# Kernel tuning notes

Measured on AMD Instinct MI355X. Metric: run time of the kernel, lower is better.

## Reference

```python
import jax, jax.numpy as jnp
import numpy as np

IMPOSSIBLE = -10000000.0
NUM_LABELS = 10
NUM_TAGS = 1 + 4 * NUM_LABELS  # 41
B, T = 4096, 256


def _bioul_constraints(num_labels):
    O, I, Bt, L, U = 0, 1, 2, 3, 4
    n = 1 + 4 * num_labels
    ft = np.ones((n, n), dtype=bool)
    ft[O, O] = False
    for i in range(num_labels):
        S = 4 * i
        for j in range(num_labels):
            SJ = 4 * j
            ft[L + S, Bt + SJ] = False
            ft[L + S, U + SJ] = False
            ft[U + S, Bt + SJ] = False
            ft[U + S, U + SJ] = False
        ft[O, Bt + S] = False
        ft[Bt + S, I + S] = False
        ft[I + S, I + S] = False
        ft[I + S, L + S] = False
        ft[Bt + S, L + S] = False
        ft[L + S, O] = False
        ft[O, U + S] = False
        ft[U + S, O] = False
    sft = np.zeros(n, dtype=bool)
    eft = np.zeros(n, dtype=bool)
    for i in range(num_labels):
        S = 4 * i
        sft[I + S] = True   # cannot start inside an entity
        sft[L + S] = True
        eft[I + S] = True   # cannot end inside an entity
        eft[Bt + S] = True
    return jnp.asarray(ft), jnp.asarray(sft), jnp.asarray(eft)


def setup_inputs() -> dict:
    key = jax.random.key(0)
    k1, k2, k3, k4, k5 = jax.random.split(key, 5)
    emissions = jax.random.normal(k1, (B, T, NUM_TAGS), dtype=jnp.float32)
    # left-aligned valid prefixes, as required by masked_flip semantics
    lengths = jax.random.randint(k2, (B,), T // 2, T + 1)
    mask = jnp.arange(T)[None, :] < lengths[:, None]
    # gold path: everything tagged O (tag 0) -- a valid BIOUL sequence
    target = jnp.zeros((B, T, NUM_TAGS), dtype=bool).at[:, :, 0].set(True)
    transitions = jax.random.normal(k3, (NUM_TAGS, NUM_TAGS), dtype=jnp.float32) * 0.1
    start_transitions = jax.random.normal(k4, (NUM_TAGS,), dtype=jnp.float32) * 0.1
    end_transitions = jax.random.normal(k5, (NUM_TAGS,), dtype=jnp.float32) * 0.1
    ft, sft, eft = _bioul_constraints(NUM_LABELS)
    return {
        "emissions": emissions,
        "mask": mask,
        "target": target,
        "transitions": transitions,
        "start_transitions": start_transitions,
        "end_transitions": end_transitions,
        "forbidden_transitions": ft,
        "start_forbidden_transitions": sft,
        "end_forbidden_transitions": eft,
    }


def _crf_loss(emissions, mask, target, transitions, start_transitions,
              end_transitions, ft, sft, eft):
    trans = jnp.where(ft, IMPOSSIBLE, transitions)           # [n, n]
    start = jnp.where(sft, IMPOSSIBLE, start_transitions)    # [n]
    end = jnp.where(eft, IMPOSSIBLE, end_transitions)        # [n]
    # supervised (target-restricted) and unsupervised emission scores
    sup = jnp.where(target, emissions, IMPOSSIBLE)           # [B, T, n]
    bi = jnp.stack([sup, emissions], axis=1)                 # [B, 2, T, n]
    bi = jnp.swapaxes(bi, 0, 2)                              # [T, 2, B, n]
    init = bi[0] + start                                     # [2, B, n]

    def step(prev, e_k):
        # logsumexp_reduce: alpha'[j] = logsumexp_i(alpha[i] + trans[i, j]) + e_k[j]
        nxt = jax.nn.logsumexp(prev[..., :, None] + trans, axis=-2) + e_k
        return nxt, nxt

    _, outs = jax.lax.scan(step, init, bi[1:])
    out = jnp.concatenate([init[None], outs], axis=0)        # [T, 2, B, n]
    out = jnp.swapaxes(out, 0, 2)                            # [B, 2, T, n]
    # masked_flip(...)[:, :, 0] == alpha at the last valid token
    lengths = mask.sum(-1)                                   # [B]
    idx = (lengths - 1)[:, None, None, None]
    z = jnp.take_along_axis(out, idx, axis=2)[:, :, 0] + end # [B, 2, n]
    supervised_z = jax.nn.logsumexp(z[:, 0], axis=-1)
    unsupervised_z = jax.nn.logsumexp(z[:, 1], axis=-1)
    return -(supervised_z - unsupervised_z)                  # [B]


def reference(emissions, mask, target, transitions, start_transitions,
              end_transitions, forbidden_transitions,
              start_forbidden_transitions, end_forbidden_transitions):
    return _crf_loss(emissions, mask, target, transitions, start_transitions,
                     end_transitions, forbidden_transitions,
                     start_forbidden_transitions, end_forbidden_transitions)
```

## Files before the change

### kernel.cpp

```cpp
#include <hip/hip_runtime.h>
#include <stdint.h>

#define NT 41
#define TT 256

typedef __attribute__((ext_vector_type(8))) short short8;
typedef __attribute__((ext_vector_type(16))) float f32x16;
typedef __attribute__((ext_vector_type(2))) int int2v;

union FragU { short8 s; uint32_t u[4]; };

static __device__ __forceinline__ uint32_t pk_bf16(float lo, float hi) {
    uint32_t d;
    asm("v_cvt_pk_bf16_f32 %0, %1, %2" : "=v"(d) : "v"(lo), "v"(hi));
    return d;
}
static __device__ __forceinline__ float asf(int x){ return __builtin_bit_cast(float, x); }
static __device__ __forceinline__ int   asi(float x){ return __builtin_bit_cast(int, x); }

static __device__ __forceinline__ float hsum(float x) {
    int2v r = __builtin_amdgcn_permlane32_swap(asi(x), asi(x), false, false);
    return asf(r[0]) + asf(r[1]);
}
static __device__ __forceinline__ uint32_t dpp_pairswap(uint32_t v) {
    return (uint32_t)__builtin_amdgcn_update_dpp(0, (int)v, 0xB1, 0xF, 0xF, true);
}
static __device__ __forceinline__ uint32_t u4c(uint4 v, int q) {
    return q==0 ? v.x : q==1 ? v.y : q==2 ? v.z : v.w;
}
static __device__ __forceinline__ short8 packB(const float* g) {
    FragU u;
    u.u[0] = pk_bf16(g[0], g[1]); u.u[1] = pk_bf16(g[2], g[3]);
    u.u[2] = pk_bf16(g[4], g[5]); u.u[3] = pk_bf16(g[6], g[7]);
    return u.s;
}

template<bool BYTE>
static __device__ __forceinline__ uint32_t bAt(const void* p, size_t idx) {
    if (BYTE) return (uint32_t)((const uint8_t*)p)[idx];
    return (((const uint32_t*)p)[idx] != 0u) ? 1u : 0u;
}

static __device__ __forceinline__ int rowOf(int rr, int h) {
    return (rr < 16) ? ((rr & 3) + 8 * (rr >> 2) + 4 * h)
                     : (32 + ((rr - 16) & 3) + 8 * ((rr - 16) >> 2) + 4 * h);
}

template<bool BYTE>
static __device__ void run_all(const float* __restrict__ em, const void* __restrict__ maskp,
    const void* __restrict__ tgtp, const float* __restrict__ trans,
    const float* __restrict__ st, const float* __restrict__ en,
    const void* __restrict__ ftp, const void* __restrict__ sftp,
    const void* __restrict__ eftp, float* __restrict__ out)
{
    __shared__ float sB[21][64];
    __shared__ float sLb[64];

    const int tid  = threadIdx.x;
    const int wid  = tid >> 6;
    const int lane = tid & 63;
    const int c = lane & 31;
    const int h = lane >> 5;
    const int bbase = blockIdx.x * 16;
    const int b = bbase + (c >> 1);
    const bool sup = ((c & 1) == 0);
    const size_t eb0 = (size_t)b * TT * NT;

    int len = 0;
    if (BYTE) {
        const uint8_t* mr = (const uint8_t*)maskp + (size_t)b * TT;
        #pragma unroll
        for (int k = 0; k < 16; ++k) {
            uint4 v; __builtin_memcpy(&v, mr + k*16, 16);
            len += __popc(v.x)+__popc(v.y)+__popc(v.z)+__popc(v.w);
        }
    } else {
        const uint32_t* mr = (const uint32_t*)maskp + (size_t)b * TT;
        for (int k = 0; k < TT; k += 4) {
            uint4 v; __builtin_memcpy(&v, mr + k, 16);
            len += (v.x!=0)+(v.y!=0)+(v.z!=0)+(v.w!=0);
        }
    }
    int tm = len;
    #pragma unroll
    for (int o = 1; o < 64; o <<= 1) { int t2 = __shfl_xor(tm, o); tm = t2 > tm ? t2 : tm; }

    float w[3][21];
    uint4 S[3][5]; uint32_t S40[3];
    const char* myrow = sup ? (const char*)(em + eb0)
                            : (const char*)tgtp + eb0 * 4;

    auto issueSlot = [&](int sl, int t) {
        const char* rp = myrow + (size_t)t * (NT * 4);
        #pragma unroll
        for (int m = 0; m < 5; ++m) {
            const int off = 4 * ((m < 4) ? (8*m + 4*h) : (32 + 4*h));
            uint4 tmp; __builtin_memcpy(&tmp, rp + off, 16);
            S[sl][m] = tmp;
        }
        uint32_t t40; __builtin_memcpy(&t40, rp + 160, 4);
        S40[sl] = t40;
    };
    auto convSlot = [&](int sl) {
        #pragma unroll
        for (int rr = 0; rr < 21; ++rr) {
            uint32_t mine = (rr < 20) ? u4c(S[sl][rr>>2], rr & 3) : S40[sl];
            uint32_t oth  = dpp_pairswap(mine);
            uint32_t embits = sup ? mine : oth;
            uint32_t tgbits = sup ? oth  : mine;
            float e = __expf(__builtin_bit_cast(float, embits));
            w[sl][rr] = ((!sup) || (tgbits != 0u)) ? e : 0.0f;
        }
    };
    auto loadStageB = [&](int s, int t) {
        const float* base = em + eb0 + (size_t)t * NT;
        float ev[21];
        #pragma unroll
        for (int m = 0; m < 5; ++m) {
            const int off = (m < 4) ? (8*m + 4*h) : (32 + 4*h);
            float4 tmp; __builtin_memcpy(&tmp, base + off, 16);
            ev[4*m+0]=tmp.x; ev[4*m+1]=tmp.y; ev[4*m+2]=tmp.z; ev[4*m+3]=tmp.w;
        }
        ev[20] = base[40];
        const uint32_t om = sup ? 0u : 0x01010101u;
        uint32_t tw[5]; uint32_t t40;
        const uint8_t* tb = (const uint8_t*)tgtp + eb0 + (size_t)t * NT;
        #pragma unroll
        for (int m = 0; m < 5; ++m) {
            const int off = (m < 4) ? (8*m + 4*h) : (32 + 4*h);
            uint32_t w_; __builtin_memcpy(&w_, tb + off, 4);
            tw[m] = w_ | om;
        }
        t40 = (((uint32_t)tb[40]) | om) & 0xffu;
        #pragma unroll
        for (int rr = 0; rr < 20; ++rr)
            w[s][rr] = __expf(ev[rr]) * (float)((tw[rr>>2] >> (8*(rr&3))) & 0xffu);
        w[s][20] = __expf(ev[20]) * (float)t40;
    };

    float aD[21];
    float logSf = 0.0f;
    const f32x16 z16 = (f32x16)0.0f;

    if (wid == 0) {
        short8 A0[3], A1[3];
        #pragma unroll
        for (int mb = 0; mb < 2; ++mb)
        #pragma unroll
        for (int ch = 0; ch < 3; ++ch) {
            float v[8];
            #pragma unroll
            for (int e = 0; e < 8; ++e) {
                const int src = (e&3) + 8*(e>>2) + 4*h + 16*ch;
                const int j = mb*32 + c;
                float val = 0.0f;
                if (src < NT && j < NT && bAt<BYTE>(ftp, src*NT + j) == 0u)
                    val = __expf(trans[src*NT + j]);
                v[e] = val;
            }
            FragU u; u.u[0]=pk_bf16(v[0],v[1]); u.u[1]=pk_bf16(v[2],v[3]);
            u.u[2]=pk_bf16(v[4],v[5]); u.u[3]=pk_bf16(v[6],v[7]);
            if (mb==0) A0[ch]=u.s; else A1[ch]=u.s;
        }

        #pragma unroll
        for (int rr = 0; rr < 21; ++rr) {
            const int row = rowOf(rr, h);
            float val = 0.0f;
            if (row < NT) {
                float wv = __expf(em[eb0 + row]);
                if (sup) wv *= (bAt<BYTE>(tgtp, eb0 + row) ? 1.0f : 0.0f);
                const float se = (bAt<BYTE>(sftp, row) == 0u) ? __expf(st[row]) : 0.0f;
                val = wv * se;
            }
            aD[rr] = val;
        }
        short8 B0 = packB(aD+0), B1 = packB(aD+8);
        short8 B2;
        { float tl[8] = {aD[16],aD[17],aD[18],aD[19],aD[20],0,0,0}; B2 = packB(tl); }

        if (BYTE) { loadStageB(0,1); loadStageB(1,2); loadStageB(2,3); }
        else      { issueSlot(0,1); issueSlot(1,2); issueSlot(2,3); convSlot(0); }

        for (int tb = 1; tb <= 127; tb += 3) {
            #pragma unroll
            for (int s = 0; s < 3; ++s) {
                const int t = tb + s;
                if (t <= 127) {
                    if (!BYTE) issueSlot(s, t + 3);
                    f32x16 d0 = __builtin_amdgcn_mfma_f32_32x32x16_bf16(A0[0], B0, z16, 0,0,0);
                    d0 = __builtin_amdgcn_mfma_f32_32x32x16_bf16(A0[1], B1, d0, 0,0,0);
                    d0 = __builtin_amdgcn_mfma_f32_32x32x16_bf16(A0[2], B2, d0, 0,0,0);
                    f32x16 d1 = __builtin_amdgcn_mfma_f32_32x32x16_bf16(A1[0], B0, z16, 0,0,0);
                    d1 = __builtin_amdgcn_mfma_f32_32x32x16_bf16(A1[1], B1, d1, 0,0,0);
                    d1 = __builtin_amdgcn_mfma_f32_32x32x16_bf16(A1[2], B2, d1, 0,0,0);
                    #pragma unroll
                    for (int rr = 0; rr < 16; ++rr) aD[rr] = d0[rr] * w[s][rr];
                    #pragma unroll
                    for (int rr = 0; rr < 4; ++rr) aD[16+rr] = d1[rr] * w[s][16+rr];
                    aD[20] = d1[4] * w[s][20];
                    if ((t & 7) == 0) {
                        float cs = 0.0f;
                        #pragma unroll
                        for (int rr = 0; rr < 21; ++rr) cs += aD[rr];
                        cs = hsum(cs); cs = fmaxf(cs, 1e-30f);
                        const float rinv = 1.0f / cs;
                        logSf += __logf(cs);
                        #pragma unroll
                        for (int rr = 0; rr < 21; ++rr) aD[rr] *= rinv;
                    }
                    B0 = packB(aD+0); B1 = packB(aD+8);
                    float tl[8] = {aD[16],aD[17],aD[18],aD[19],aD[20],0,0,0};
                    B2 = packB(tl);
                    if (BYTE) loadStageB(s, t + 3);
                    else      convSlot((s + 1) % 3);
                }
            }
        }
    } else {
        short8 A0[3], A1[3];
        #pragma unroll
        for (int mb = 0; mb < 2; ++mb)
        #pragma unroll
        for (int ch = 0; ch < 3; ++ch) {
            float v[8];
            #pragma unroll
            for (int e = 0; e < 8; ++e) {
                const int src = (e&3) + 8*(e>>2) + 4*h + 16*ch;
                const int i = mb*32 + c;
                float val = 0.0f;
                if (src < NT && i < NT && bAt<BYTE>(ftp, i*NT + src) == 0u)
                    val = __expf(trans[i*NT + src]);
                v[e] = val;
            }
            FragU u; u.u[0]=pk_bf16(v[0],v[1]); u.u[1]=pk_bf16(v[2],v[3]);
            u.u[2]=pk_bf16(v[4],v[5]); u.u[3]=pk_bf16(v[6],v[7]);
            if (mb==0) A0[ch]=u.s; else A1[ch]=u.s;
        }

        float endD[21];
        #pragma unroll
        for (int rr = 0; rr < 21; ++rr) {
            const int row = rowOf(rr, h);
            endD[rr] = (row < NT && bAt<BYTE>(eftp, row) == 0u) ? __expf(en[row]) : 0.0f;
        }

        short8 G0 = {0,0,0,0,0,0,0,0}, G1 = {0,0,0,0,0,0,0,0}, G2 = {0,0,0,0,0,0,0,0};
        float logSb = 0.0f;

        if (BYTE) { loadStageB(0, tm-1); loadStageB(1, tm-2); loadStageB(2, tm-3); }
        else      { issueSlot(0, tm-1); issueSlot(1, tm-2); issueSlot(2, tm-3); convSlot(0); }

        for (int tb = tm - 1; tb >= 128; tb -= 3) {
            #pragma unroll
            for (int s = 0; s < 3; ++s) {
                const int t = tb - s;
                if (t >= 128) {
                    if (!BYTE) issueSlot(s, t - 3);
                    f32x16 d0 = __builtin_amdgcn_mfma_f32_32x32x16_bf16(A0[0], G0, z16, 0,0,0);
                    d0 = __builtin_amdgcn_mfma_f32_32x32x16_bf16(A0[1], G1, d0, 0,0,0);
                    d0 = __builtin_amdgcn_mfma_f32_32x32x16_bf16(A0[2], G2, d0, 0,0,0);
                    f32x16 d1 = __builtin_amdgcn_mfma_f32_32x32x16_bf16(A1[0], G0, z16, 0,0,0);
                    d1 = __builtin_amdgcn_mfma_f32_32x32x16_bf16(A1[1], G1, d1, 0,0,0);
                    d1 = __builtin_amdgcn_mfma_f32_32x32x16_bf16(A1[2], G2, d1, 0,0,0);
                    const bool sel = (len - 1 == t);
                    float gD[21];
                    #pragma unroll
                    for (int rr = 0; rr < 16; ++rr) gD[rr] = (sel ? endD[rr] : d0[rr]) * w[s][rr];
                    #pragma unroll
                    for (int rr = 0; rr < 4; ++rr) gD[16+rr] = (sel ? endD[16+rr] : d1[rr]) * w[s][16+rr];
                    gD[20] = (sel ? endD[20] : d1[4]) * w[s][20];
                    if ((t & 7) == 0) {
                        float cs = 0.0f;
                        #pragma unroll
                        for (int rr = 0; rr < 21; ++rr) cs += gD[rr];
                        cs = hsum(cs);
                        const bool started = (len - 1 >= t);
                        const float csc = fmaxf(cs, 1e-30f);
                        const float rinv = started ? (1.0f / csc) : 1.0f;
                        logSb += started ? __logf(csc) : 0.0f;
                        #pragma unroll
                        for (int rr = 0; rr < 21; ++rr) gD[rr] *= rinv;
                    }
                    G0 = packB(gD+0); G1 = packB(gD+8);
                    float tl[8] = {gD[16],gD[17],gD[18],gD[19],gD[20],0,0,0};
                    G2 = packB(tl);
                    if (BYTE) loadStageB(s, t - 3);
                    else      convSlot((s + 1) % 3);
                }
            }
        }

        f32x16 d0 = __builtin_amdgcn_mfma_f32_32x32x16_bf16(A0[0], G0, z16, 0,0,0);
        d0 = __builtin_amdgcn_mfma_f32_32x32x16_bf16(A0[1], G1, d0, 0,0,0);
        d0 = __builtin_amdgcn_mfma_f32_32x32x16_bf16(A0[2], G2, d0, 0,0,0);
        f32x16 d1 = __builtin_amdgcn_mfma_f32_32x32x16_bf16(A1[0], G0, z16, 0,0,0);
        d1 = __builtin_amdgcn_mfma_f32_32x32x16_bf16(A1[1], G1, d1, 0,0,0);
        d1 = __builtin_amdgcn_mfma_f32_32x32x16_bf16(A1[2], G2, d1, 0,0,0);
        const bool sel = (len - 1 == 127);
        #pragma unroll
        for (int rr = 0; rr < 16; ++rr) sB[rr][lane] = sel ? endD[rr] : d0[rr];
        #pragma unroll
        for (int rr = 0; rr < 4; ++rr) sB[16+rr][lane] = sel ? endD[16+rr] : d1[rr];
        sB[20][lane] = sel ? endD[20] : d1[4];
        sLb[lane] = logSb;
    }

    __syncthreads();

    if (wid == 0) {
        float es = 0.0f;
        #pragma unroll
        for (int rr = 0; rr < 21; ++rr) es = fmaf(aD[rr], sB[rr][lane], es);
        es = hsum(es);
        const float zc = __logf(fmaxf(es, 1e-37f)) + logSf + sLb[lane];
        const float zo = __shfl_xor(zc, 1);
        if ((lane & 1) == 0 && lane < 32)
            out[bbase + (lane >> 1)] = zo - zc;
    }
}

__global__ __launch_bounds__(128, 1) void crf_fb(
    const float* __restrict__ em, const void* __restrict__ maskp,
    const void* __restrict__ tgtp, const float* __restrict__ trans,
    const float* __restrict__ st, const float* __restrict__ en,
    const void* __restrict__ ftp, const void* __restrict__ sftp,
    const void* __restrict__ eftp, float* __restrict__ out)
{
    const bool byteMode = (*(const uint32_t*)maskp == 0x01010101u);
    if (byteMode) run_all<true >(em, maskp, tgtp, trans, st, en, ftp, sftp, eftp, out);
    else          run_all<false>(em, maskp, tgtp, trans, st, en, ftp, sftp, eftp, out);
}

extern "C" void kernel_launch(void* const* d_in, const int* in_sizes, int n_in,
                              void* d_out, int out_size, void* d_ws, size_t ws_size,
                              hipStream_t stream) {
    const float* em    = (const float*)d_in[0];
    const void*  maskp = d_in[1];
    const void*  tgtp  = d_in[2];
    const float* trans = (const float*)d_in[3];
    const float* st    = (const float*)d_in[4];
    const float* en    = (const float*)d_in[5];
    const void*  ftp   = d_in[6];
    const void*  sftp  = d_in[7];
    const void*  eftp  = d_in[8];
    float* out = (float*)d_out;

    crf_fb<<<4096 / 16, 128, 0, stream>>>(em, maskp, tgtp, trans, st, en,
                                          ftp, sftp, eftp, out);
}
```

Before: 128.0 us.

## Stage emission/target prefetch through LDS via global_load_lds instead of registers

Replaces the register-held three-slot prefetch of emission and target rows with direct global-to-LDS loads into a four-slot shared-memory ring per wave, tracked with explicit vmcnt waits. Each step reads its slot from LDS and computes the exp weights just before the MFMA chain rather than after it. This is meant to cut VGPR pressure from the in-flight prefetch buffers and the per-slot weight arrays. In exchange it adds LDS traffic and depends on a hand-counted vmcnt threshold, and the byte path now loads synchronously inside the step instead of being prefetched three steps ahead.

```diff
diff --git a/kernel.cpp b/kernel.cpp
--- a/kernel.cpp
+++ b/kernel.cpp
@@ -3,6 +3,7 @@
 
 #define NT 41
 #define TT 256
+#define SLOT_U4 336
 
 typedef __attribute__((ext_vector_type(8))) short short8;
 typedef __attribute__((ext_vector_type(16))) float f32x16;
@@ -24,9 +25,6 @@
 }
 static __device__ __forceinline__ uint32_t dpp_pairswap(uint32_t v) {
     return (uint32_t)__builtin_amdgcn_update_dpp(0, (int)v, 0xB1, 0xF, 0xF, true);
-}
-static __device__ __forceinline__ uint32_t u4c(uint4 v, int q) {
-    return q==0 ? v.x : q==1 ? v.y : q==2 ? v.z : v.w;
 }
 static __device__ __forceinline__ short8 packB(const float* g) {
     FragU u;
@@ -53,6 +51,7 @@
     const void* __restrict__ ftp, const void* __restrict__ sftp,
     const void* __restrict__ eftp, float* __restrict__ out)
 {
+    __shared__ uint4 stage[2][4][SLOT_U4];
     __shared__ float sB[21][64];
     __shared__ float sLb[64];
 
@@ -85,34 +84,51 @@
     #pragma unroll
     for (int o = 1; o < 64; o <<= 1) { int t2 = __shfl_xor(tm, o); tm = t2 > tm ? t2 : tm; }
 
-    float w[3][21];
-    uint4 S[3][5]; uint32_t S40[3];
     const char* myrow = sup ? (const char*)(em + eb0)
                             : (const char*)tgtp + eb0 * 4;
+    uint4* mystage = &stage[wid][0][0];
 
     auto issueSlot = [&](int sl, int t) {
         const char* rp = myrow + (size_t)t * (NT * 4);
+        uint4* slotb = mystage + sl * SLOT_U4;
         #pragma unroll
         for (int m = 0; m < 5; ++m) {
             const int off = 4 * ((m < 4) ? (8*m + 4*h) : (32 + 4*h));
-            uint4 tmp; __builtin_memcpy(&tmp, rp + off, 16);
-            S[sl][m] = tmp;
-        }
-        uint32_t t40; __builtin_memcpy(&t40, rp + 160, 4);
-        S40[sl] = t40;
+            __builtin_amdgcn_global_load_lds(
+                (const __attribute__((address_space(1))) uint32_t*)(rp + off),
+                (__attribute__((address_space(3))) uint32_t*)(slotb + m * 64),
+                16, 0, 0);
+        }
+        __builtin_amdgcn_global_load_lds(
+            (const __attribute__((address_space(1))) uint32_t*)(rp + 160),
+            (__attribute__((address_space(3))) uint32_t*)((uint32_t*)slotb + 1280),
+            4, 0, 0);
     };
-    auto convSlot = [&](int sl) {
+
+    uint32_t mine[21];
+    auto ldSlot = [&](int sl) {
+        asm volatile("s_waitcnt vmcnt(12)" ::: "memory");
+        __builtin_amdgcn_sched_barrier(0);
+        const uint4* slotb = mystage + sl * SLOT_U4;
+        #pragma unroll
+        for (int m = 0; m < 5; ++m) {
+            uint4 v = slotb[m * 64 + lane];
+            mine[4*m+0]=v.x; mine[4*m+1]=v.y; mine[4*m+2]=v.z; mine[4*m+3]=v.w;
+        }
+        mine[20] = ((const uint32_t*)slotb)[1280 + lane];
+    };
+    float w[21];
+    auto mkW = [&]() {
         #pragma unroll
         for (int rr = 0; rr < 21; ++rr) {
-            uint32_t mine = (rr < 20) ? u4c(S[sl][rr>>2], rr & 3) : S40[sl];
-            uint32_t oth  = dpp_pairswap(mine);
-            uint32_t embits = sup ? mine : oth;
-            uint32_t tgbits = sup ? oth  : mine;
+            uint32_t oth = dpp_pairswap(mine[rr]);
+            uint32_t embits = sup ? mine[rr] : oth;
+            uint32_t tgbits = sup ? oth : mine[rr];
             float e = __expf(__builtin_bit_cast(float, embits));
-            w[sl][rr] = ((!sup) || (tgbits != 0u)) ? e : 0.0f;
+            w[rr] = ((!sup) || (tgbits != 0u)) ? e : 0.0f;
         }
     };
-    auto loadStageB = [&](int s, int t) {
+    auto loadStageB = [&](int t) {
         const float* base = em + eb0 + (size_t)t * NT;
         float ev[21];
         #pragma unroll
@@ -134,8 +150,8 @@
         t40 = (((uint32_t)tb[40]) | om) & 0xffu;
         #pragma unroll
         for (int rr = 0; rr < 20; ++rr)
-            w[s][rr] = __expf(ev[rr]) * (float)((tw[rr>>2] >> (8*(rr&3))) & 0xffu);
-        w[s][20] = __expf(ev[20]) * (float)t40;
+            w[rr] = __expf(ev[rr]) * (float)((tw[rr>>2] >> (8*(rr&3))) & 0xffu);
+        w[20] = __expf(ev[20]) * (float)t40;
     };
 
     float aD[21];
@@ -163,6 +179,8 @@
             if (mb==0) A0[ch]=u.s; else A1[ch]=u.s;
         }
 
+        if (!BYTE) { issueSlot(1 & 3, 1); issueSlot(2 & 3, 2); issueSlot(3 & 3, 3); }
+
         #pragma unroll
         for (int rr = 0; rr < 21; ++rr) {
             const int row = rowOf(rr, h);
@@ -179,15 +197,18 @@
         short8 B2;
         { float tl[8] = {aD[16],aD[17],aD[18],aD[19],aD[20],0,0,0}; B2 = packB(tl); }
 
-        if (BYTE) { loadStageB(0,1); loadStageB(1,2); loadStageB(2,3); }
-        else      { issueSlot(0,1); issueSlot(1,2); issueSlot(2,3); convSlot(0); }
-
         for (int tb = 1; tb <= 127; tb += 3) {
             #pragma unroll
             for (int s = 0; s < 3; ++s) {
                 const int t = tb + s;
                 if (t <= 127) {
-                    if (!BYTE) issueSlot(s, t + 3);
+                    if (!BYTE) {
+                        ldSlot(t & 3);
+                        issueSlot((t + 3) & 3, t + 3);
+                        mkW();
+                    } else {
+                        loadStageB(t);
+                    }
                     f32x16 d0 = __builtin_amdgcn_mfma_f32_32x32x16_bf16(A0[0], B0, z16, 0,0,0);
                     d0 = __builtin_amdgcn_mfma_f32_32x32x16_bf16(A0[1], B1, d0, 0,0,0);
                     d0 = __builtin_amdgcn_mfma_f32_32x32x16_bf16(A0[2], B2, d0, 0,0,0);
@@ -195,10 +216,10 @@
                     d1 = __builtin_amdgcn_mfma_f32_32x32x16_bf16(A1[1], B1, d1, 0,0,0);
                     d1 = __builtin_amdgcn_mfma_f32_32x32x16_bf16(A1[2], B2, d1, 0,0,0);
                     #pragma unroll
-                    for (int rr = 0; rr < 16; ++rr) aD[rr] = d0[rr] * w[s][rr];
+                    for (int rr = 0; rr < 16; ++rr) aD[rr] = d0[rr] * w[rr];
                     #pragma unroll
-                    for (int rr = 0; rr < 4; ++rr) aD[16+rr] = d1[rr] * w[s][16+rr];
-                    aD[20] = d1[4] * w[s][20];
+                    for (int rr = 0; rr < 4; ++rr) aD[16+rr] = d1[rr] * w[16+rr];
+                    aD[20] = d1[4] * w[20];
                     if ((t & 7) == 0) {
                         float cs = 0.0f;
                         #pragma unroll
@@ -212,8 +233,6 @@
                     B0 = packB(aD+0); B1 = packB(aD+8);
                     float tl[8] = {aD[16],aD[17],aD[18],aD[19],aD[20],0,0,0};
                     B2 = packB(tl);
-                    if (BYTE) loadStageB(s, t + 3);
-                    else      convSlot((s + 1) % 3);
                 }
             }
         }
@@ -248,15 +267,20 @@
         short8 G0 = {0,0,0,0,0,0,0,0}, G1 = {0,0,0,0,0,0,0,0}, G2 = {0,0,0,0,0,0,0,0};
         float logSb = 0.0f;
 
-        if (BYTE) { loadStageB(0, tm-1); loadStageB(1, tm-2); loadStageB(2, tm-3); }
-        else      { issueSlot(0, tm-1); issueSlot(1, tm-2); issueSlot(2, tm-3); convSlot(0); }
+        if (!BYTE) { issueSlot((tm-1) & 3, tm-1); issueSlot((tm-2) & 3, tm-2); issueSlot((tm-3) & 3, tm-3); }
 
         for (int tb = tm - 1; tb >= 128; tb -= 3) {
             #pragma unroll
             for (int s = 0; s < 3; ++s) {
                 const int t = tb - s;
                 if (t >= 128) {
-                    if (!BYTE) issueSlot(s, t - 3);
+                    if (!BYTE) {
+                        ldSlot(t & 3);
+                        issueSlot((t - 3) & 3, t - 3);
+                        mkW();
+                    } else {
+                        loadStageB(t);
+                    }
                     f32x16 d0 = __builtin_amdgcn_mfma_f32_32x32x16_bf16(A0[0], G0, z16, 0,0,0);
                     d0 = __builtin_amdgcn_mfma_f32_32x32x16_bf16(A0[1], G1, d0, 0,0,0);
                     d0 = __builtin_amdgcn_mfma_f32_32x32x16_bf16(A0[2], G2, d0, 0,0,0);
@@ -266,10 +290,10 @@
                     const bool sel = (len - 1 == t);
                     float gD[21];
                     #pragma unroll
-                    for (int rr = 0; rr < 16; ++rr) gD[rr] = (sel ? endD[rr] : d0[rr]) * w[s][rr];
+                    for (int rr = 0; rr < 16; ++rr) gD[rr] = (sel ? endD[rr] : d0[rr]) * w[rr];
                     #pragma unroll
-                    for (int rr = 0; rr < 4; ++rr) gD[16+rr] = (sel ? endD[16+rr] : d1[rr]) * w[s][16+rr];
-                    gD[20] = (sel ? endD[20] : d1[4]) * w[s][20];
+                    for (int rr = 0; rr < 4; ++rr) gD[16+rr] = (sel ? endD[16+rr] : d1[rr]) * w[16+rr];
+                    gD[20] = (sel ? endD[20] : d1[4]) * w[20];
                     if ((t & 7) == 0) {
                         float cs = 0.0f;
                         #pragma unroll
@@ -285,8 +309,6 @@
                     G0 = packB(gD+0); G1 = packB(gD+8);
                     float tl[8] = {gD[16],gD[17],gD[18],gD[19],gD[20],0,0,0};
                     G2 = packB(tl);
-                    if (BYTE) loadStageB(s, t - 3);
-                    else      convSlot((s + 1) % 3);
                 }
             }
         }
```

Result: slower. 137.3 us (+7.3%).

## Split CRF recurrence into six parallel time segments combined by matrix products

Applied to the files above, without the earlier changes.

Replaces the two-wave forward/backward split of the 256-step recurrence with six waves, each running a 64-step segment. Some waves propagate state vectors and others propagate ones-vectors through transfer products. A final combine step stitches the segment results together using dot products and one extra MFMA, with a branch per length bucket. The goal is to shorten the serial dependency chain per batch group from about 128 steps to about 64. The cost is more total work, more waves per block, extra register pressure and a more complex combine with different bf16 rounding behavior.

```diff
diff --git a/kernel.cpp b/kernel.cpp
--- a/kernel.cpp
+++ b/kernel.cpp
@@ -17,7 +17,6 @@
 }
 static __device__ __forceinline__ float asf(int x){ return __builtin_bit_cast(float, x); }
 static __device__ __forceinline__ int   asi(float x){ return __builtin_bit_cast(int, x); }
-
 static __device__ __forceinline__ float hsum(float x) {
     int2v r = __builtin_amdgcn_permlane32_swap(asi(x), asi(x), false, false);
     return asf(r[0]) + asf(r[1]);
@@ -28,22 +27,175 @@
 static __device__ __forceinline__ uint32_t u4c(uint4 v, int q) {
     return q==0 ? v.x : q==1 ? v.y : q==2 ? v.z : v.w;
 }
-static __device__ __forceinline__ short8 packB(const float* g) {
+static __device__ __forceinline__ short8 packB8(const float* g) {
     FragU u;
     u.u[0] = pk_bf16(g[0], g[1]); u.u[1] = pk_bf16(g[2], g[3]);
     u.u[2] = pk_bf16(g[4], g[5]); u.u[3] = pk_bf16(g[6], g[7]);
     return u.s;
 }
-
+static __device__ __forceinline__ short8 packTail(const float* g) {
+    float tl[8] = {g[0], g[1], g[2], g[3], g[4], 0.f, 0.f, 0.f};
+    return packB8(tl);
+}
 template<bool BYTE>
 static __device__ __forceinline__ uint32_t bAt(const void* p, size_t idx) {
     if (BYTE) return (uint32_t)((const uint8_t*)p)[idx];
     return (((const uint32_t*)p)[idx] != 0u) ? 1u : 0u;
 }
-
 static __device__ __forceinline__ int rowOf(int rr, int h) {
     return (rr < 16) ? ((rr & 3) + 8 * (rr >> 2) + 4 * h)
                      : (32 + ((rr - 16) & 3) + 8 * ((rr - 16) >> 2) + 4 * h);
+}
+static __device__ __forceinline__ void mfma6(const short8* A, short8 B0, short8 B1, short8 B2,
+                                             float* d ) {
+    const f32x16 z16 = (f32x16)0.0f;
+    f32x16 d0 = __builtin_amdgcn_mfma_f32_32x32x16_bf16(A[0], B0, z16, 0,0,0);
+    d0 = __builtin_amdgcn_mfma_f32_32x32x16_bf16(A[1], B1, d0, 0,0,0);
+    d0 = __builtin_amdgcn_mfma_f32_32x32x16_bf16(A[2], B2, d0, 0,0,0);
+    f32x16 d1 = __builtin_amdgcn_mfma_f32_32x32x16_bf16(A[3], B0, z16, 0,0,0);
+    d1 = __builtin_amdgcn_mfma_f32_32x32x16_bf16(A[4], B1, d1, 0,0,0);
+    d1 = __builtin_amdgcn_mfma_f32_32x32x16_bf16(A[5], B2, d1, 0,0,0);
+    #pragma unroll
+    for (int rr = 0; rr < 16; ++rr) d[rr] = d0[rr];
+    #pragma unroll
+    for (int rr = 0; rr < 5; ++rr) d[16+rr] = d1[rr];
+}
+
+template<bool BYTE>
+static __device__ void buildA(bool fwd, int c, int h, const float* trans,
+                              const void* ftp, short8* A) {
+    #pragma unroll
+    for (int mb = 0; mb < 2; ++mb)
+    #pragma unroll
+    for (int ch = 0; ch < 3; ++ch) {
+        float v[8];
+        #pragma unroll
+        for (int e = 0; e < 8; ++e) {
+            const int src = (e&3) + 8*(e>>2) + 4*h + 16*ch;
+            const int o = mb*32 + c;
+            const int i_ = fwd ? src : o;
+            const int j_ = fwd ? o : src;
+            float val = 0.0f;
+            if (src < NT && o < NT && bAt<BYTE>(ftp, i_*NT + j_) == 0u)
+                val = __expf(trans[i_*NT + j_]);
+            v[e] = val;
+        }
+        FragU u; u.u[0]=pk_bf16(v[0],v[1]); u.u[1]=pk_bf16(v[2],v[3]);
+        u.u[2]=pk_bf16(v[4],v[5]); u.u[3]=pk_bf16(v[6],v[7]);
+        A[mb*3 + ch] = u.s;
+    }
+}
+
+template<bool BYTE, int N, bool ASC, bool PRE, bool REINIT>
+static __device__ float run_pass(int t0, int len, bool sup, int h,
+    const char* myrow, const float* emb, const uint8_t* tgb8,
+    const short8* A, const float* endD, float aD[21])
+{
+    float w[3][21];
+    uint4 S[3][5]; uint32_t S40[3];
+
+    auto tAt = [&](int i){ return ASC ? (t0 + i) : (t0 - i); };
+    auto issueSlot = [&](int sl, int t) {
+        const char* rp = myrow + (size_t)t * (NT * 4);
+        #pragma unroll
+        for (int m = 0; m < 5; ++m) {
+            const int off = 4 * ((m < 4) ? (8*m + 4*h) : (32 + 4*h));
+            uint4 tmp; __builtin_memcpy(&tmp, rp + off, 16);
+            S[sl][m] = tmp;
+        }
+        uint32_t t40; __builtin_memcpy(&t40, rp + 160, 4);
+        S40[sl] = t40;
+    };
+    auto convSlot = [&](int sl) {
+        #pragma unroll
+        for (int rr = 0; rr < 21; ++rr) {
+            uint32_t mine = (rr < 20) ? u4c(S[sl][rr>>2], rr & 3) : S40[sl];
+            uint32_t oth = dpp_pairswap(mine);
+            uint32_t embits = sup ? mine : oth;
+            uint32_t tgbits = sup ? oth : mine;
+            float e = __expf(__builtin_bit_cast(float, embits));
+            w[sl][rr] = ((!sup) || (tgbits != 0u)) ? e : 0.0f;
+        }
+    };
+    auto loadB = [&](int sl, int t) {
+        const float* base = emb + (size_t)t * NT;
+        const uint8_t* tb = tgb8 + (size_t)t * NT;
+        const uint32_t om = sup ? 0u : 0x01010101u;
+        float ev[21]; uint32_t tw[5]; uint32_t t40;
+        #pragma unroll
+        for (int m = 0; m < 5; ++m) {
+            const int off = (m < 4) ? (8*m + 4*h) : (32 + 4*h);
+            float4 tmp; __builtin_memcpy(&tmp, base + off, 16);
+            ev[4*m+0]=tmp.x; ev[4*m+1]=tmp.y; ev[4*m+2]=tmp.z; ev[4*m+3]=tmp.w;
+            uint32_t w_; __builtin_memcpy(&w_, tb + off, 4);
+            tw[m] = w_ | om;
+        }
+        ev[20] = base[40];
+        t40 = (((uint32_t)tb[40]) | om) & 0xffu;
+        #pragma unroll
+        for (int rr = 0; rr < 20; ++rr)
+            w[sl][rr] = __expf(ev[rr]) * (float)((tw[rr>>2] >> (8*(rr&3))) & 0xffu);
+        w[sl][20] = __expf(ev[20]) * (float)t40;
+    };
+
+    if (!BYTE) {
+        issueSlot(0, tAt(0)); issueSlot(1, tAt(1)); issueSlot(2, tAt(2));
+        convSlot(0);
+    } else {
+        loadB(0, tAt(0));
+    }
+
+    float logS = 0.0f;
+    constexpr int NB3 = (N + 2) / 3;
+    for (int bb = 0; bb < NB3; ++bb) {
+        #pragma unroll
+        for (int s = 0; s < 3; ++s) {
+            const int i = bb * 3 + s;
+            if (i < N) {
+                if (!BYTE) { if (i + 3 < N) issueSlot(s, tAt(i + 3)); }
+                const int t = tAt(i);
+                short8 B0, B1, B2;
+                if (PRE) {
+                    float tmp[21];
+                    #pragma unroll
+                    for (int rr = 0; rr < 21; ++rr) tmp[rr] = aD[rr] * w[s][rr];
+                    B0 = packB8(tmp); B1 = packB8(tmp+8); B2 = packTail(tmp+16);
+                } else {
+                    B0 = packB8(aD); B1 = packB8(aD+8); B2 = packTail(aD+16);
+                }
+                float d[21]; mfma6(A, B0, B1, B2, d);
+                if (PRE) {
+                    #pragma unroll
+                    for (int rr = 0; rr < 21; ++rr) aD[rr] = d[rr];
+                } else if (REINIT) {
+                    const bool sel = (len - 1 == t);
+                    #pragma unroll
+                    for (int rr = 0; rr < 21; ++rr)
+                        aD[rr] = (sel ? endD[rr] : d[rr]) * w[s][rr];
+                } else {
+                    #pragma unroll
+                    for (int rr = 0; rr < 21; ++rr) aD[rr] = d[rr] * w[s][rr];
+                }
+                if ((t & 7) == 0) {
+                    const bool started = (!REINIT) || (len - 1 >= t);
+                    float cs = 0.0f;
+                    #pragma unroll
+                    for (int rr = 0; rr < 21; ++rr) cs += aD[rr];
+                    cs = hsum(cs);
+                    const float csc = fmaxf(cs, 1e-30f);
+                    const float rinv = started ? (1.0f / csc) : 1.0f;
+                    logS += started ? __logf(csc) : 0.0f;
+                    #pragma unroll
+                    for (int rr = 0; rr < 21; ++rr) aD[rr] *= rinv;
+                }
+                if (i + 1 < N) {
+                    if (BYTE) loadB((s + 1) % 3, tAt(i + 1));
+                    else      convSlot((s + 1) % 3);
+                }
+            }
+        }
+    }
+    return logS;
 }
 
 template<bool BYTE>
@@ -53,8 +205,8 @@
     const void* __restrict__ ftp, const void* __restrict__ sftp,
     const void* __restrict__ eftp, float* __restrict__ out)
 {
-    __shared__ float sB[21][64];
-    __shared__ float sLb[64];
+    __shared__ float sb[6][21][64];
+    __shared__ float ssig[6][64];
 
     const int tid  = threadIdx.x;
     const int wid  = tid >> 6;
@@ -81,88 +233,29 @@
             len += (v.x!=0)+(v.y!=0)+(v.z!=0)+(v.w!=0);
         }
     }
-    int tm = len;
-    #pragma unroll
-    for (int o = 1; o < 64; o <<= 1) { int t2 = __shfl_xor(tm, o); tm = t2 > tm ? t2 : tm; }
-
-    float w[3][21];
-    uint4 S[3][5]; uint32_t S40[3];
+
     const char* myrow = sup ? (const char*)(em + eb0)
                             : (const char*)tgtp + eb0 * 4;
-
-    auto issueSlot = [&](int sl, int t) {
-        const char* rp = myrow + (size_t)t * (NT * 4);
-        #pragma unroll
-        for (int m = 0; m < 5; ++m) {
-            const int off = 4 * ((m < 4) ? (8*m + 4*h) : (32 + 4*h));
-            uint4 tmp; __builtin_memcpy(&tmp, rp + off, 16);
-            S[sl][m] = tmp;
-        }
-        uint32_t t40; __builtin_memcpy(&t40, rp + 160, 4);
-        S40[sl] = t40;
-    };
-    auto convSlot = [&](int sl) {
-        #pragma unroll
-        for (int rr = 0; rr < 21; ++rr) {
-            uint32_t mine = (rr < 20) ? u4c(S[sl][rr>>2], rr & 3) : S40[sl];
-            uint32_t oth  = dpp_pairswap(mine);
-            uint32_t embits = sup ? mine : oth;
-            uint32_t tgbits = sup ? oth  : mine;
-            float e = __expf(__builtin_bit_cast(float, embits));
-            w[sl][rr] = ((!sup) || (tgbits != 0u)) ? e : 0.0f;
-        }
-    };
-    auto loadStageB = [&](int s, int t) {
-        const float* base = em + eb0 + (size_t)t * NT;
-        float ev[21];
-        #pragma unroll
-        for (int m = 0; m < 5; ++m) {
-            const int off = (m < 4) ? (8*m + 4*h) : (32 + 4*h);
-            float4 tmp; __builtin_memcpy(&tmp, base + off, 16);
-            ev[4*m+0]=tmp.x; ev[4*m+1]=tmp.y; ev[4*m+2]=tmp.z; ev[4*m+3]=tmp.w;
-        }
-        ev[20] = base[40];
-        const uint32_t om = sup ? 0u : 0x01010101u;
-        uint32_t tw[5]; uint32_t t40;
-        const uint8_t* tb = (const uint8_t*)tgtp + eb0 + (size_t)t * NT;
-        #pragma unroll
-        for (int m = 0; m < 5; ++m) {
-            const int off = (m < 4) ? (8*m + 4*h) : (32 + 4*h);
-            uint32_t w_; __builtin_memcpy(&w_, tb + off, 4);
-            tw[m] = w_ | om;
-        }
-        t40 = (((uint32_t)tb[40]) | om) & 0xffu;
-        #pragma unroll
-        for (int rr = 0; rr < 20; ++rr)
-            w[s][rr] = __expf(ev[rr]) * (float)((tw[rr>>2] >> (8*(rr&3))) & 0xffu);
-        w[s][20] = __expf(ev[20]) * (float)t40;
-    };
+    const float*  emb  = em + eb0;
+    const uint8_t* tgb8 = (const uint8_t*)tgtp + eb0;
+
+    const bool isFwdA = (wid == 0 || wid == 1 || wid == 5);
+    short8 A[6];
+    buildA<BYTE>(isFwdA, c, h, trans, ftp, A);
+
+    float endD[21];
+    if (wid == 3 || wid == 4) {
+        #pragma unroll
+        for (int rr = 0; rr < 21; ++rr) {
+            const int row = rowOf(rr, h);
+            endD[rr] = (row < NT && bAt<BYTE>(eftp, row) == 0u) ? __expf(en[row]) : 0.0f;
+        }
+    }
 
     float aD[21];
-    float logSf = 0.0f;
-    const f32x16 z16 = (f32x16)0.0f;
+    float sig = 0.0f;
 
     if (wid == 0) {
-        short8 A0[3], A1[3];
-        #pragma unroll
-        for (int mb = 0; mb < 2; ++mb)
-        #pragma unroll
-        for (int ch = 0; ch < 3; ++ch) {
-            float v[8];
-            #pragma unroll
-            for (int e = 0; e < 8; ++e) {
-                const int src = (e&3) + 8*(e>>2) + 4*h + 16*ch;
-                const int j = mb*32 + c;
-                float val = 0.0f;
-                if (src < NT && j < NT && bAt<BYTE>(ftp, src*NT + j) == 0u)
-                    val = __expf(trans[src*NT + j]);
-                v[e] = val;
-            }
-            FragU u; u.u[0]=pk_bf16(v[0],v[1]); u.u[1]=pk_bf16(v[2],v[3]);
-            u.u[2]=pk_bf16(v[4],v[5]); u.u[3]=pk_bf16(v[6],v[7]);
-            if (mb==0) A0[ch]=u.s; else A1[ch]=u.s;
-        }
-
         #pragma unroll
         for (int rr = 0; rr < 21; ++rr) {
             const int row = rowOf(rr, h);
@@ -175,152 +268,82 @@
             }
             aD[rr] = val;
         }
-        short8 B0 = packB(aD+0), B1 = packB(aD+8);
-        short8 B2;
-        { float tl[8] = {aD[16],aD[17],aD[18],aD[19],aD[20],0,0,0}; B2 = packB(tl); }
-
-        if (BYTE) { loadStageB(0,1); loadStageB(1,2); loadStageB(2,3); }
-        else      { issueSlot(0,1); issueSlot(1,2); issueSlot(2,3); convSlot(0); }
-
-        for (int tb = 1; tb <= 127; tb += 3) {
-            #pragma unroll
-            for (int s = 0; s < 3; ++s) {
-                const int t = tb + s;
-                if (t <= 127) {
-                    if (!BYTE) issueSlot(s, t + 3);
-                    f32x16 d0 = __builtin_amdgcn_mfma_f32_32x32x16_bf16(A0[0], B0, z16, 0,0,0);
-                    d0 = __builtin_amdgcn_mfma_f32_32x32x16_bf16(A0[1], B1, d0, 0,0,0);
-                    d0 = __builtin_amdgcn_mfma_f32_32x32x16_bf16(A0[2], B2, d0, 0,0,0);
-                    f32x16 d1 = __builtin_amdgcn_mfma_f32_32x32x16_bf16(A1[0], B0, z16, 0,0,0);
-                    d1 = __builtin_amdgcn_mfma_f32_32x32x16_bf16(A1[1], B1, d1, 0,0,0);
-                    d1 = __builtin_amdgcn_mfma_f32_32x32x16_bf16(A1[2], B2, d1, 0,0,0);
-                    #pragma unroll
-                    for (int rr = 0; rr < 16; ++rr) aD[rr] = d0[rr] * w[s][rr];
-                    #pragma unroll
-                    for (int rr = 0; rr < 4; ++rr) aD[16+rr] = d1[rr] * w[s][16+rr];
-                    aD[20] = d1[4] * w[s][20];
-                    if ((t & 7) == 0) {
-                        float cs = 0.0f;
-                        #pragma unroll
-                        for (int rr = 0; rr < 21; ++rr) cs += aD[rr];
-                        cs = hsum(cs); cs = fmaxf(cs, 1e-30f);
-                        const float rinv = 1.0f / cs;
-                        logSf += __logf(cs);
-                        #pragma unroll
-                        for (int rr = 0; rr < 21; ++rr) aD[rr] *= rinv;
-                    }
-                    B0 = packB(aD+0); B1 = packB(aD+8);
-                    float tl[8] = {aD[16],aD[17],aD[18],aD[19],aD[20],0,0,0};
-                    B2 = packB(tl);
-                    if (BYTE) loadStageB(s, t + 3);
-                    else      convSlot((s + 1) % 3);
-                }
-            }
-        }
+        sig = run_pass<BYTE,63,true,false,false>(1, len, sup, h, myrow, emb, tgb8, A, endD, aD);
+    } else if (wid == 1) {
+        #pragma unroll
+        for (int rr = 0; rr < 21; ++rr) aD[rr] = (rowOf(rr,h) < NT) ? 1.0f : 0.0f;
+        sig = run_pass<BYTE,64,true,false,false>(64, len, sup, h, myrow, emb, tgb8, A, endD, aD);
+    } else if (wid == 2) {
+        #pragma unroll
+        for (int rr = 0; rr < 21; ++rr) aD[rr] = (rowOf(rr,h) < NT) ? 1.0f : 0.0f;
+        sig = run_pass<BYTE,64,false,true,false>(127, len, sup, h, myrow, emb, tgb8, A, endD, aD);
+    } else if (wid == 3) {
+        #pragma unroll
+        for (int rr = 0; rr < 21; ++rr) aD[rr] = 0.0f;
+        sig = run_pass<BYTE,64,false,false,true>(255, len, sup, h, myrow, emb, tgb8, A, endD, aD);
+    } else if (wid == 4) {
+        #pragma unroll
+        for (int rr = 0; rr < 21; ++rr) aD[rr] = (rowOf(rr,h) < NT) ? 1.0f : 0.0f;
+        sig = run_pass<BYTE,64,false,false,true>(191, len, sup, h, myrow, emb, tgb8, A, endD, aD);
     } else {
-        short8 A0[3], A1[3];
-        #pragma unroll
-        for (int mb = 0; mb < 2; ++mb)
-        #pragma unroll
-        for (int ch = 0; ch < 3; ++ch) {
-            float v[8];
-            #pragma unroll
-            for (int e = 0; e < 8; ++e) {
-                const int src = (e&3) + 8*(e>>2) + 4*h + 16*ch;
-                const int i = mb*32 + c;
-                float val = 0.0f;
-                if (src < NT && i < NT && bAt<BYTE>(ftp, i*NT + src) == 0u)
-                    val = __expf(trans[i*NT + src]);
-                v[e] = val;
-            }
-            FragU u; u.u[0]=pk_bf16(v[0],v[1]); u.u[1]=pk_bf16(v[2],v[3]);
-            u.u[2]=pk_bf16(v[4],v[5]); u.u[3]=pk_bf16(v[6],v[7]);
-            if (mb==0) A0[ch]=u.s; else A1[ch]=u.s;
-        }
-
-        float endD[21];
+        #pragma unroll
+        for (int rr = 0; rr < 21; ++rr) aD[rr] = (rowOf(rr,h) < NT) ? 1.0f : 0.0f;
+        sig = run_pass<BYTE,64,true,true,false>(128, len, sup, h, myrow, emb, tgb8, A, endD, aD);
+    }
+
+    #pragma unroll
+    for (int rr = 0; rr < 21; ++rr) sb[wid][rr][lane] = aD[rr];
+    ssig[wid][lane] = sig;
+
+    __syncthreads();
+
+    if (wid == 0) {
+        float endC[21];
         #pragma unroll
         for (int rr = 0; rr < 21; ++rr) {
             const int row = rowOf(rr, h);
-            endD[rr] = (row < NT && bAt<BYTE>(eftp, row) == 0u) ? __expf(en[row]) : 0.0f;
-        }
-
-        short8 G0 = {0,0,0,0,0,0,0,0}, G1 = {0,0,0,0,0,0,0,0}, G2 = {0,0,0,0,0,0,0,0};
-        float logSb = 0.0f;
-
-        if (BYTE) { loadStageB(0, tm-1); loadStageB(1, tm-2); loadStageB(2, tm-3); }
-        else      { issueSlot(0, tm-1); issueSlot(1, tm-2); issueSlot(2, tm-3); convSlot(0); }
-
-        for (int tb = tm - 1; tb >= 128; tb -= 3) {
-            #pragma unroll
-            for (int s = 0; s < 3; ++s) {
-                const int t = tb - s;
-                if (t >= 128) {
-                    if (!BYTE) issueSlot(s, t - 3);
-                    f32x16 d0 = __builtin_amdgcn_mfma_f32_32x32x16_bf16(A0[0], G0, z16, 0,0,0);
-                    d0 = __builtin_amdgcn_mfma_f32_32x32x16_bf16(A0[1], G1, d0, 0,0,0);
-                    d0 = __builtin_amdgcn_mfma_f32_32x32x16_bf16(A0[2], G2, d0, 0,0,0);
-                    f32x16 d1 = __builtin_amdgcn_mfma_f32_32x32x16_bf16(A1[0], G0, z16, 0,0,0);
-                    d1 = __builtin_amdgcn_mfma_f32_32x32x16_bf16(A1[1], G1, d1, 0,0,0);
-                    d1 = __builtin_amdgcn_mfma_f32_32x32x16_bf16(A1[2], G2, d1, 0,0,0);
-                    const bool sel = (len - 1 == t);
-                    float gD[21];
-                    #pragma unroll
-                    for (int rr = 0; rr < 16; ++rr) gD[rr] = (sel ? endD[rr] : d0[rr]) * w[s][rr];
-                    #pragma unroll
-                    for (int rr = 0; rr < 4; ++rr) gD[16+rr] = (sel ? endD[16+rr] : d1[rr]) * w[s][16+rr];
-                    gD[20] = (sel ? endD[20] : d1[4]) * w[s][20];
-                    if ((t & 7) == 0) {
-                        float cs = 0.0f;
-                        #pragma unroll
-                        for (int rr = 0; rr < 21; ++rr) cs += gD[rr];
-                        cs = hsum(cs);
-                        const bool started = (len - 1 >= t);
-                        const float csc = fmaxf(cs, 1e-30f);
-                        const float rinv = started ? (1.0f / csc) : 1.0f;
-                        logSb += started ? __logf(csc) : 0.0f;
-                        #pragma unroll
-                        for (int rr = 0; rr < 21; ++rr) gD[rr] *= rinv;
-                    }
-                    G0 = packB(gD+0); G1 = packB(gD+8);
-                    float tl[8] = {gD[16],gD[17],gD[18],gD[19],gD[20],0,0,0};
-                    G2 = packB(tl);
-                    if (BYTE) loadStageB(s, t - 3);
-                    else      convSlot((s + 1) % 3);
-                }
-            }
-        }
-
-        f32x16 d0 = __builtin_amdgcn_mfma_f32_32x32x16_bf16(A0[0], G0, z16, 0,0,0);
-        d0 = __builtin_amdgcn_mfma_f32_32x32x16_bf16(A0[1], G1, d0, 0,0,0);
-        d0 = __builtin_amdgcn_mfma_f32_32x32x16_bf16(A0[2], G2, d0, 0,0,0);
-        f32x16 d1 = __builtin_amdgcn_mfma_f32_32x32x16_bf16(A1[0], G0, z16, 0,0,0);
-        d1 = __builtin_amdgcn_mfma_f32_32x32x16_bf16(A1[1], G1, d1, 0,0,0);
-        d1 = __builtin_amdgcn_mfma_f32_32x32x16_bf16(A1[2], G2, d1, 0,0,0);
-        const bool sel = (len - 1 == 127);
-        #pragma unroll
-        for (int rr = 0; rr < 16; ++rr) sB[rr][lane] = sel ? endD[rr] : d0[rr];
-        #pragma unroll
-        for (int rr = 0; rr < 4; ++rr) sB[16+rr][lane] = sel ? endD[16+rr] : d1[rr];
-        sB[20][lane] = sel ? endD[20] : d1[4];
-        sLb[lane] = logSb;
-    }
-
-    __syncthreads();
-
-    if (wid == 0) {
-        float es = 0.0f;
-        #pragma unroll
-        for (int rr = 0; rr < 21; ++rr) es = fmaf(aD[rr], sB[rr][lane], es);
-        es = hsum(es);
-        const float zc = __logf(fmaxf(es, 1e-37f)) + logSf + sLb[lane];
+            endC[rr] = (row < NT && bAt<BYTE>(eftp, row) == 0u) ? __expf(en[row]) : 0.0f;
+        }
+        float yB[21], g4[21];
+        float d1=0.f, d2=0.f, d3=0.f, d4=0.f, d5e=0.f;
+        #pragma unroll
+        for (int rr = 0; rr < 21; ++rr) {
+            const int row = rowOf(rr, h);
+            const float uv = (row < NT) ? 1.0f : 0.0f;
+            const float a63 = sb[0][rr][lane];
+            const float zB  = sb[2][rr][lane];
+            yB[rr]          = sb[1][rr][lane];
+            const float g9  = sb[3][rr][lane];
+            g4[rr]          = sb[4][rr][lane];
+            const float z2  = sb[5][rr][lane];
+            d1 += zB * a63; d2 += yB[rr] * uv; d3 += z2 * g9;
+            d4 += g4[rr] * uv; d5e += yB[rr] * endC[rr];
+        }
+        d1 = hsum(d1); d2 = hsum(d2); d3 = hsum(d3); d4 = hsum(d4); d5e = hsum(d5e);
+
+        short8 B0 = packB8(yB), B1 = packB8(yB+8), B2 = packTail(yB+16);
+        float ey[21]; mfma6(A, B0, B1, B2, ey);
+        float d5 = 0.f;
+        #pragma unroll
+        for (int rr = 0; rr < 21; ++rr) d5 += ey[rr] * g4[rr];
+        d5 = hsum(d5);
+
+        const float sA = ssig[0][lane], szv = ssig[2][lane];
+        const float s3 = ssig[3][lane], s4 = ssig[4][lane], s5 = ssig[5][lane];
+        const float base = szv + sA + __logf(fmaxf(d1, 1e-37f)) - __logf(fmaxf(d2, 1e-37f));
+        const float l5  = __logf(fmaxf(d5, 1e-37f));
+        const float tail =
+            (len == 128) ? __logf(fmaxf(d5e, 1e-37f))
+          : (len <= 192) ? (l5 + s4)
+          : (l5 + s3 + s5 + __logf(fmaxf(d3, 1e-37f)) - __logf(fmaxf(d4, 1e-37f)));
+        const float zc = base + tail;
         const float zo = __shfl_xor(zc, 1);
         if ((lane & 1) == 0 && lane < 32)
             out[bbase + (lane >> 1)] = zo - zc;
     }
 }
 
-__global__ __launch_bounds__(128, 1) void crf_fb(
+__global__ __launch_bounds__(384) void crf_seg(
     const float* __restrict__ em, const void* __restrict__ maskp,
     const void* __restrict__ tgtp, const float* __restrict__ trans,
     const float* __restrict__ st, const float* __restrict__ en,
@@ -346,6 +369,6 @@
     const void*  eftp  = d_in[8];
     float* out = (float*)d_out;
 
-    crf_fb<<<4096 / 16, 128, 0, stream>>>(em, maskp, tgtp, trans, st, en,
-                                          ftp, sftp, eftp, out);
-}
+    crf_seg<<<4096 / 16, 384, 0, stream>>>(em, maskp, tgtp, trans, st, en,
+                                           ftp, sftp, eftp, out);
+}
```

New measurement: 136.0 us. 6.3% more time.
